# Kernel optimization log

Measured on AMD Instinct MI355X. Metric: run time of the kernel, lower is better.

The kernel has to match this reference:

```python
import jax, jax.numpy as jnp
import numpy as np

EPS = 1e-3  # keras LayerNormalization default epsilon

def _ln(x, gamma, beta):
    m = jnp.mean(x, axis=-1, keepdims=True)
    v = jnp.var(x, axis=-1, keepdims=True)
    return gamma * (x - m) * jax.lax.rsqrt(v + EPS) + beta

def setup_inputs() -> dict:
    B, T, F, H = 256, 128, 4, 512  # T*F must equal H (skip-connection constraint in context GRN)
    D = T * F
    key = jax.random.key(0)
    ks = jax.random.split(key, 16)
    s = lambda fan: 1.0 / np.sqrt(fan)
    inp = {
        "inputs": jax.random.normal(ks[0], (B, T, F), jnp.float32),
        # context GRN (input dim D = T*F = H)
        "W1c": jax.random.normal(ks[1], (D, H), jnp.float32) * s(D),
        "b1c": jnp.zeros((H,), jnp.float32),
        "W2c": jax.random.normal(ks[2], (H, H), jnp.float32) * s(H),
        "b2c": jnp.zeros((H,), jnp.float32),
        "Wgc": jax.random.normal(ks[3], (H, H), jnp.float32) * s(H),
        "bgc": jnp.zeros((H,), jnp.float32),
        "gamma_c": jnp.ones((H,), jnp.float32),
        "beta_c": jnp.zeros((H,), jnp.float32),
        # softmax variable-selection head
        "Wsel": jax.random.normal(ks[4], (H, F), jnp.float32) * s(H),
        "bsel": jnp.zeros((F,), jnp.float32),
        # F per-variable GRNs, batched over leading F axis (input dim 1)
        "w1": jax.random.normal(ks[5], (F, H), jnp.float32),
        "b1": jnp.zeros((F, H), jnp.float32),
        "W2": jax.random.normal(ks[6], (F, H, H), jnp.float32) * s(H),
        "b2": jnp.zeros((F, H), jnp.float32),
        "Wg": jax.random.normal(ks[7], (F, H, H), jnp.float32) * s(H),
        "bg": jnp.zeros((F, H), jnp.float32),
        "gamma": jnp.ones((F, H), jnp.float32),
        "beta": jnp.zeros((F, H), jnp.float32),
    }
    return inp

def reference(inputs, W1c, b1c, W2c, b2c, Wgc, bgc, gamma_c, beta_c,
              Wsel, bsel, w1, b1, W2, b2, Wg, bg, gamma, beta):
    B, T, F = inputs.shape
    # ---- context GRN on flattened inputs (skip == flat since T*F == H) ----
    flat = inputs.reshape(B, T * F)
    x = jax.nn.elu(flat @ W1c + b1c)
    x = x @ W2c + b2c
    g = jax.nn.sigmoid(x @ Wgc + bgc)
    ctx = _ln(g * x + (1.0 - g) * flat, gamma_c, beta_c)
    # ---- softmax selection weights over variables ----
    sel = jax.nn.softmax(ctx @ Wsel + bsel)  # [B, F]
    # ---- per-variable GRNs, batched over F (input is scalar per variable) ----
    v = inputs[..., None]                              # [B,T,F,1] (skip path)
    x1 = jax.nn.elu(v * w1 + b1)                       # [B,T,F,H]
    x2 = jnp.einsum('btfh,fhk->btfk', x1, W2) + b2     # dense2
    gv = jax.nn.sigmoid(jnp.einsum('btfh,fhk->btfk', x2, Wg) + bg)
    gated = gv * x2 + (1.0 - gv) * v                   # skip broadcasts [B,T,F,1]
    tv = _ln(gated, gamma, beta)                       # [B,T,F,H]
    # ---- weighted sum over variables ----
    selected = jnp.einsum('btfh,bf->bth', tv, sel)     # [B,T,H]
    sel_weights = jnp.tile(sel[:, None, None, :], (1, T, 1, 1))  # [B,T,1,F]
    return selected, sel_weights
```

## Files before the change

### kernel.cpp

```cpp
#include <hip/hip_runtime.h>
#include <math.h>


#define H 512
#define NF 4
#define MTOT 32768

typedef unsigned short u16;
typedef unsigned int u32;
typedef __attribute__((ext_vector_type(8))) short short8;
typedef __attribute__((ext_vector_type(4))) float f32x4;
typedef __attribute__((ext_vector_type(4))) u32 u32x4;

__device__ __forceinline__ u16 f2bf(float x) {
  union { float f; u32 u; } v; v.f = x;
  return (u16)((v.u + 0x7fffu + ((v.u >> 16) & 1u)) >> 16);
}
__device__ __forceinline__ float bf2f(u32 h16) {
  union { u32 u; float f; } v; v.u = h16 << 16;
  return v.f;
}
__device__ __forceinline__ float elu_f(float x) {
  return x > 0.0f ? x : (__expf(x) - 1.0f);
}
__device__ __forceinline__ float sigmoid_f(float x) {
  return __builtin_amdgcn_rcpf(1.0f + __expf(-x));
}
__device__ __forceinline__ u32 cvtpk(float lo, float hi) {
  u32 r;
  asm("v_cvt_pk_bf16_f32 %0, %1, %2" : "=v"(r) : "v"(lo), "v"(hi));
  return r;
}
template <int CTRL>
__device__ __forceinline__ float dppadd(float v) {
  int t = __builtin_amdgcn_update_dpp(0, __float_as_int(v), CTRL, 0xF, 0xF, true);
  return v + __int_as_float(t);
}
__device__ __forceinline__ float red16(float v) {
  v = dppadd<0xB1>(v);
  v = dppadd<0x4E>(v);
  v = dppadd<0x141>(v);
  v = dppadd<0x140>(v);
  return v;
}

__device__ __forceinline__ void glld16(const void* g, void* l) {
  __builtin_amdgcn_global_load_lds(
      (const __attribute__((address_space(1))) u32*)(unsigned long long)(uintptr_t)g,
      (__attribute__((address_space(3))) u32*)(u32)(uintptr_t)l, 16, 0, 0);
}

#define MFMA16(a, b, c) __builtin_amdgcn_mfma_f32_16x16x32_bf16((a), (b), (c), 0, 0, 0)

__device__ __forceinline__ int sA_idx(int m, int n) {
  return m * 512 + ((((n >> 3) ^ (m & 7)) << 3) + (n & 7));
}

struct TileCtx {
  int tid, wid, lane, quad, col;
};

__global__ __launch_bounds__(256)
void pack_vsn(const float* __restrict__ W2, const float* __restrict__ Wg,
              u16* __restrict__ W2p, u16* __restrict__ Wgp) {
  int g = blockIdx.x * 256 + threadIdx.x;
  int r = g & 32767; int mat = g >> 15;
  int lane = r & 63, nt = (r >> 6) & 31, kk = (r >> 11) & 15;
  const float* src; u16* dst;
  if (mat < 4) { src = W2 + (size_t)mat * 262144;       dst = W2p + (size_t)mat * 262144; }
  else         { src = Wg + (size_t)(mat - 4) * 262144; dst = Wgp + (size_t)(mat - 4) * 262144; }
  dst += (size_t)r * 8;
  int n  = nt * 16 + (lane & 15);
  int k0 = kk * 32 + (lane >> 4) * 8;
  short8 pk;
  #pragma unroll
  for (int j = 0; j < 8; ++j) pk[j] = (short)f2bf(src[(size_t)(k0 + j) * H + n]);
  *(short8*)dst = pk;
}

__global__ __launch_bounds__(256)
void pack_ctx(const float* __restrict__ W1c, const float* __restrict__ W2c,
              const float* __restrict__ Wgc, u16* __restrict__ Cp) {
  int g = blockIdx.x * 256 + threadIdx.x;
  int r = g & 32767; int mat = g >> 15;
  const float* src = (mat == 0) ? W1c : (mat == 1) ? W2c : Wgc;
  u16* dst = Cp + (size_t)mat * 262144 + (size_t)r * 8;
  int lane = r & 63;
  int n, k0;
  if (mat < 2) {
    int nb = r >> 12, kk = (r >> 8) & 15, ntg = (r >> 6) & 3;
    n  = nb * 64 + ntg * 16 + (lane & 15);
    k0 = kk * 32 + (lane >> 4) * 8;
  } else {
    int nt = (r >> 6) & 31, kk = (r >> 11) & 15;
    n  = nt * 16 + (lane & 15);
    k0 = kk * 32 + (lane >> 4) * 8;
  }
  short8 pk;
  #pragma unroll
  for (int j = 0; j < 8; ++j) pk[j] = (short)f2bf(src[(size_t)(k0 + j) * H + n]);
  *(short8*)dst = pk;
}


__device__ __forceinline__ void slab_kloop(const TileCtx& c, const u16* Wslab,
                                           u16* sA, u16* sB0, u16* sB1,
                                           f32x4 acc[4]) {
  #pragma unroll 1
  for (int kk = 0; kk < 16; ++kk) {
    if (kk < 15)
      glld16(Wslab + (kk + 1) * 2048 + c.tid * 8,
             (((kk + 1) & 1) ? sB1 : sB0) + c.tid * 8);
    const u16* bp = ((kk & 1) ? sB1 : sB0) + c.wid * 512 + c.lane * 8;
    short8 bb = *(const short8*)(bp);
    const int kq = kk * 4 + c.quad;
    const int s0 = (kq ^ (c.col & 7)) * 8;
    short8 a0 = *(const short8*)&sA[(     c.col) * 512 + s0];
    short8 a1 = *(const short8*)&sA[(16 + c.col) * 512 + s0];
    short8 a2 = *(const short8*)&sA[(32 + c.col) * 512 + s0];
    short8 a3 = *(const short8*)&sA[(48 + c.col) * 512 + s0];
    acc[0] = MFMA16(a0, bb, acc[0]);
    acc[1] = MFMA16(a1, bb, acc[1]);
    acc[2] = MFMA16(a2, bb, acc[2]);
    acc[3] = MFMA16(a3, bb, acc[3]);
    __syncthreads();
  }
}

__global__ __launch_bounds__(256)
void ctx_g1(const float* __restrict__ in, const u16* __restrict__ Cp,
            const float* __restrict__ b1c, u16* __restrict__ x1g) {
  __shared__ __align__(16) u16 smem[36864];
  u16* const sA  = smem;
  u16* const sB0 = smem + 32768;
  u16* const sB1 = smem + 34816;
  TileCtx c;
  c.tid = threadIdx.x; c.wid = c.tid >> 6; c.lane = c.tid & 63;
  c.quad = c.lane >> 4; c.col = c.lane & 15;
  const int mb = blockIdx.x >> 3, nb = blockIdx.x & 7;
  const int m0 = mb * 64;
  const u16* Wslab = Cp + (size_t)nb * 32768;

  glld16(Wslab + c.tid * 8, sB0 + c.tid * 8);

  {
    const int m = c.tid >> 2;
    const int kb = (c.tid & 3) * 128;
    const float* rowp = in + (size_t)(m0 + m) * H;
    #pragma unroll
    for (int gg = 0; gg < 16; ++gg) {
      const int ge = (gg + (c.tid & 3) * 4) & 15;
      const int k = kb + ge * 8;
      float4 v0 = *(const float4*)&rowp[k];
      float4 v1 = *(const float4*)&rowp[k + 4];
      u32x4 pk4;
      pk4.x = cvtpk(v0.x, v0.y); pk4.y = cvtpk(v0.z, v0.w);
      pk4.z = cvtpk(v1.x, v1.y); pk4.w = cvtpk(v1.z, v1.w);
      const int grp = (k >> 3) ^ (m & 7);
      *(u32x4*)&sA[m * 512 + grp * 8] = pk4;
    }
  }
  __syncthreads();

  f32x4 acc[4];
  #pragma unroll
  for (int mt = 0; mt < 4; ++mt) acc[mt] = (f32x4){0,0,0,0};
  slab_kloop(c, Wslab, sA, sB0, sB1, acc);

  const int n = nb * 64 + c.wid * 16 + c.col;
  const float bv = b1c[n];
  #pragma unroll
  for (int mt = 0; mt < 4; ++mt)
    #pragma unroll
    for (int reg = 0; reg < 4; ++reg) {
      const int m = m0 + mt * 16 + c.quad * 4 + reg;
      x1g[(size_t)m * H + n] = f2bf(elu_f(acc[mt][reg] + bv));
    }
}

__global__ __launch_bounds__(256)
void ctx_g2(const u16* __restrict__ x1g, const u16* __restrict__ Cp,
            const float* __restrict__ b2c, u16* __restrict__ xg) {
  __shared__ __align__(16) u16 smem[36864];
  u16* const sA  = smem;
  u16* const sB0 = smem + 32768;
  u16* const sB1 = smem + 34816;
  TileCtx c;
  c.tid = threadIdx.x; c.wid = c.tid >> 6; c.lane = c.tid & 63;
  c.quad = c.lane >> 4; c.col = c.lane & 15;
  const int mb = blockIdx.x >> 3, nb = blockIdx.x & 7;
  const int m0 = mb * 64;
  const u16* Wslab = Cp + 262144 + (size_t)nb * 32768;

  glld16(Wslab + c.tid * 8, sB0 + c.tid * 8);

  {
    const int m = c.tid >> 2;
    const int kb = (c.tid & 3) * 128;
    const u16* rowp = x1g + (size_t)(m0 + m) * H;
    #pragma unroll
    for (int gg = 0; gg < 16; ++gg) {
      const int ge = (gg + (c.tid & 3) * 4) & 15;
      const int k = kb + ge * 8;
      short8 w = *(const short8*)&rowp[k];
      const int grp = (k >> 3) ^ (m & 7);
      *(short8*)&sA[m * 512 + grp * 8] = w;
    }
  }
  __syncthreads();

  f32x4 acc[4];
  #pragma unroll
  for (int mt = 0; mt < 4; ++mt) acc[mt] = (f32x4){0,0,0,0};
  slab_kloop(c, Wslab, sA, sB0, sB1, acc);

  const int n = nb * 64 + c.wid * 16 + c.col;
  const float bv = b2c[n];
  #pragma unroll
  for (int mt = 0; mt < 4; ++mt)
    #pragma unroll
    for (int reg = 0; reg < 4; ++reg) {
      const int m = m0 + mt * 16 + c.quad * 4 + reg;
      xg[(size_t)m * H + n] = f2bf(acc[mt][reg] + bv);
    }
}


__device__ __forceinline__ void stage_chunk8(int tid, const u16* src, u16* dst) {
  glld16(src + tid * 8,         dst + tid * 8);
  glld16(src + tid * 8 + 4096,  dst + tid * 8 + 4096);
  glld16(src + tid * 8 + 8192,  dst + tid * 8 + 8192);
  glld16(src + tid * 8 + 12288, dst + tid * 8 + 12288);
}

template <bool PREFETCH_TAIL>
__device__ __forceinline__ void gemm_kloop8(const TileCtx& c, const u16* Wp,
                                            const u16* nextWp,
                                            u16* sA, u16* sB0, u16* sB1,
                                            f32x4 acc[4][4]) {
  #pragma unroll 1
  for (int kk = 0; kk < 16; ++kk) {
    if (kk < 15) {
      stage_chunk8(c.tid, Wp + (kk + 1) * 16384, (((kk + 1) & 1) ? sB1 : sB0));
    } else if (PREFETCH_TAIL) {
      stage_chunk8(c.tid, nextWp, sB0);
    }
    const u16* bp = ((kk & 1) ? sB1 : sB0) + c.wid * 2048 + c.lane * 8;
    short8 bb[4];
    #pragma unroll
    for (int nt = 0; nt < 4; ++nt) bb[nt] = *(const short8*)(bp + nt * 512);
    const int kq = kk * 4 + c.quad;
    const int s0 = (kq ^ (c.col & 7)) * 8;
    #pragma unroll
    for (int mt = 0; mt < 4; ++mt) {
      short8 a = *(const short8*)&sA[(mt * 16 + c.col) * 512 + s0];
      #pragma unroll
      for (int nt = 0; nt < 4; ++nt)
        acc[mt][nt] = MFMA16(a, bb[nt], acc[mt][nt]);
    }
    __syncthreads();
  }
}

__device__ __forceinline__ void store_x2_pair_n(const TileCtx& c, u16* sA,
                                                int mt, int n, u32 o01, u32 o23) {
  const bool even = (c.lane & 1) == 0;
  const u32 send = even ? o23 : o01;
  const u32 recv = (u32)__builtin_amdgcn_update_dpp(0, (int)send, 0xB1, 0xF, 0xF, true);
  const u32 hi = even ? recv : o23;
  const u32 lo = even ? o01 : recv;
  const u32 dlo = __builtin_amdgcn_perm(hi, lo, 0x05040100u);
  const u32 dhi = __builtin_amdgcn_perm(hi, lo, 0x07060302u);
  const int np = n & ~1;
  const int mA = mt * 16 + c.quad * 4 + (even ? 0 : 2);
  const int iA = mA * 512 + ((((np >> 3) ^ (mA & 7)) << 3) + (np & 7));
  const int mB = mA + 1;
  const int iB = mB * 512 + ((((np >> 3) ^ (mB & 7)) << 3) + (np & 7));
  *(u32*)&sA[iA] = dlo;
  *(u32*)&sA[iB] = dhi;
}

__device__ __forceinline__ void ln_reduce8(const TileCtx& c, float* sRedF,
                                           f32x4 acc[4][4]) {
  #pragma unroll
  for (int mt = 0; mt < 4; ++mt) {
    float rs[4], rq[4];
    #pragma unroll
    for (int reg = 0; reg < 4; ++reg) {
      rs[reg] = 0.f; rq[reg] = 0.f;
      #pragma unroll
      for (int nt = 0; nt < 4; ++nt) {
        const float gt = acc[mt][nt][reg];
        rs[reg] += gt; rq[reg] += gt * gt;
      }
      rs[reg] = red16(rs[reg]);
      rq[reg] = red16(rq[reg]);
    }
    if (c.col == 0) {
      #pragma unroll
      for (int reg = 0; reg < 4; ++reg) {
        const int m = mt * 16 + c.quad * 4 + reg;
        float2 sq; sq.x = rs[reg]; sq.y = rq[reg];
        *(float2*)&sRedF[m * 20 + c.wid * 2] = sq;
      }
    }
  }
  __syncthreads();
  if (c.tid < 64) {
    const int row = c.tid;
    float s = 0.f, q = 0.f;
    #pragma unroll
    for (int jj = 0; jj < 4; ++jj) {
      float4 v = *(float4*)&sRedF[row * 20 + jj * 4];
      s += v.x + v.z; q += v.y + v.w;
    }
    const float mu = s * (1.0f / H);
    const float rstd = rsqrtf(q * (1.0f / H) - mu * mu + 1e-3f);
    float2 mr; mr.x = mu; mr.y = rstd;
    *(float2*)&sRedF[1280 + row * 2] = mr;
  }
  __syncthreads();
}

__global__ __launch_bounds__(512)
void ctx_g3(const float* __restrict__ in, const u16* __restrict__ xg,
            const u16* __restrict__ Cp,
            const float* __restrict__ bgc,
            const float* __restrict__ gamma_c, const float* __restrict__ beta_c,
            const float* __restrict__ Wsel, const float* __restrict__ bsel,
            float* __restrict__ sel_ws,
            float* __restrict__ selw_out)
{
  __shared__ __align__(16) u16 smem[65536];
  u16* const sA  = smem;
  u16* const sB0 = smem + 32768;
  u16* const sB1 = smem + 49152;
  float* const sRedF = (float*)sB0;
  float* const sZp   = (float*)sB0 + 2048;
  float* const sZf   = (float*)sB0 + 4096;
  float* const sSel  = (float*)sB0 + 4352;

  TileCtx c;
  c.tid = threadIdx.x; c.wid = c.tid >> 6; c.lane = c.tid & 63;
  c.quad = c.lane >> 4; c.col = c.lane & 15;
  const int b0 = blockIdx.x * 64;
  const u16* Wgcp = Cp + 524288;

  stage_chunk8(c.tid, Wgcp, sB0);

  {
    const int m  = c.tid >> 3;
    const int kb = (c.tid & 7) * 64;
    const u16* rowp = xg + (size_t)(b0 + m) * H;
    #pragma unroll
    for (int gg = 0; gg < 8; ++gg) {
      const int ge = (gg + (c.tid & 7)) & 7;
      const int k = kb + ge * 8;
      short8 w = *(const short8*)&rowp[k];
      const int grp = (k >> 3) ^ (m & 7);
      *(short8*)&sA[m * 512 + grp * 8] = w;
    }
  }
  __syncthreads();

  f32x4 acc[4][4];
  #pragma unroll
  for (int mt = 0; mt < 4; ++mt)
    #pragma unroll
    for (int nt = 0; nt < 4; ++nt) acc[mt][nt] = (f32x4){0,0,0,0};
  gemm_kloop8<false>(c, Wgcp, nullptr, sA, sB0, sB1, acc);

  {
    float bv[4];
    #pragma unroll
    for (int nt = 0; nt < 4; ++nt) bv[nt] = bgc[c.wid * 64 + nt * 16 + c.col];
    #pragma unroll
    for (int mt = 0; mt < 4; ++mt)
      #pragma unroll
      for (int nt = 0; nt < 4; ++nt) {
        const int n = c.wid * 64 + nt * 16 + c.col;
        #pragma unroll
        for (int reg = 0; reg < 4; ++reg) {
          const int m = mt * 16 + c.quad * 4 + reg;
          const float xv = bf2f(sA[sA_idx(m, n)]);
          const float fl = in[(size_t)(b0 + m) * H + n];
          const float gv = sigmoid_f(acc[mt][nt][reg] + bv[nt]);
          acc[mt][nt][reg] = gv * xv + (1.0f - gv) * fl;
        }
      }
  }
  __syncthreads();
  ln_reduce8(c, sRedF, acc);

  {
    float gm[4], bt[4]; float4 ws4[4];
    #pragma unroll
    for (int nt = 0; nt < 4; ++nt) {
      const int n = c.wid * 64 + nt * 16 + c.col;
      gm[nt] = gamma_c[n]; bt[nt] = beta_c[n];
      ws4[nt] = *(const float4*)&Wsel[n * NF];
    }
    #pragma unroll
    for (int mt = 0; mt < 4; ++mt)
      #pragma unroll
      for (int reg = 0; reg < 4; ++reg) {
        const int m = mt * 16 + c.quad * 4 + reg;
        float2 mr = *(float2*)&sRedF[1280 + m * 2];
        float zp[4] = {0.f, 0.f, 0.f, 0.f};
        #pragma unroll
        for (int nt = 0; nt < 4; ++nt) {
          const float ctxv = gm[nt] * ((acc[mt][nt][reg] - mr.x) * mr.y) + bt[nt];
          zp[0] = fmaf(ctxv, ws4[nt].x, zp[0]);
          zp[1] = fmaf(ctxv, ws4[nt].y, zp[1]);
          zp[2] = fmaf(ctxv, ws4[nt].z, zp[2]);
          zp[3] = fmaf(ctxv, ws4[nt].w, zp[3]);
        }
        #pragma unroll
        for (int f = 0; f < 4; ++f) zp[f] = red16(zp[f]);
        if (c.col == 0) {
          #pragma unroll
          for (int f = 0; f < 4; ++f) sZp[(m * 8 + c.wid) * 4 + f] = zp[f];
        }
      }
  }
  __syncthreads();
  if (c.tid < 256) {
    const int m = c.tid >> 2, f = c.tid & 3;
    float z = bsel[f];
    #pragma unroll
    for (int w = 0; w < 8; ++w) z += sZp[(m * 8 + w) * 4 + f];
    sZf[m * 4 + f] = z;
  }
  __syncthreads();
  if (c.tid < 64) {
    const int m = c.tid;
    float z0 = sZf[m*4], z1 = sZf[m*4+1], z2 = sZf[m*4+2], z3 = sZf[m*4+3];
    float mx = fmaxf(fmaxf(z0, z1), fmaxf(z2, z3));
    float e0 = __expf(z0-mx), e1 = __expf(z1-mx), e2 = __expf(z2-mx), e3 = __expf(z3-mx);
    float inv = __builtin_amdgcn_rcpf(e0 + e1 + e2 + e3);
    sSel[m*4]   = e0*inv; sSel[m*4+1] = e1*inv;
    sSel[m*4+2] = e2*inv; sSel[m*4+3] = e3*inv;
    sel_ws[(b0+m)*NF]   = e0*inv; sel_ws[(b0+m)*NF+1] = e1*inv;
    sel_ws[(b0+m)*NF+2] = e2*inv; sel_ws[(b0+m)*NF+3] = e3*inv;
  }
  __syncthreads();
  {
    const int m = c.tid >> 3;
    const int jb = (c.tid & 7) * 64;
    float4 v; v.x = sSel[m*4]; v.y = sSel[m*4+1]; v.z = sSel[m*4+2]; v.w = sSel[m*4+3];
    #pragma unroll
    for (int j = 0; j < 16; ++j)
      *(float4*)&selw_out[(size_t)(b0 + m) * H + jb + j * 4] = v;
  }
}

__global__ __launch_bounds__(512, 2)
void vsn_mfma(const float* __restrict__ in,
              const float* __restrict__ w1, const float* __restrict__ b1,
              const float* __restrict__ b2, const float* __restrict__ bg,
              const float* __restrict__ gamma, const float* __restrict__ beta,
              const u16* __restrict__ W2p, const u16* __restrict__ Wgp,
              const float* __restrict__ sel_ws,
              float* __restrict__ out)
{
  __shared__ __align__(16) u16 smem[65536];
  u16* const sA  = smem;
  u16* const sB0 = smem + 32768;
  u16* const sB1 = smem + 49152;
  float* const sRedF = (float*)smem;

  TileCtx c;
  c.tid = threadIdx.x; c.wid = c.tid >> 6; c.lane = c.tid & 63;
  c.quad = c.lane >> 4; c.col = c.lane & 15;
  const int row0 = blockIdx.x * 64;
  const int bidx = row0 >> 7;

  f32x4 outacc[4][4];
  #pragma unroll
  for (int mt = 0; mt < 4; ++mt)
    #pragma unroll
    for (int nt = 0; nt < 4; ++nt) outacc[mt][nt] = (f32x4){0,0,0,0};

  stage_chunk8(c.tid, W2p, sB0);

  #pragma unroll 1
  for (int f = 0; f < NF; ++f) {
    const u16* W2f = W2p + (size_t)f * 262144;
    const u16* Wgf = Wgp + (size_t)f * 262144;
    const u16* W2n = W2p + (size_t)((f + 1) & 3) * 262144;

    {
      const int m  = c.tid >> 3;
      const int kb = (c.tid & 7) * 64;
      const float v = in[(size_t)(row0 + m) * NF + f];
      const float* w1f = w1 + f * H;
      const float* b1f = b1 + f * H;
      #pragma unroll
      for (int gg = 0; gg < 8; ++gg) {
        const int ge = (gg + (c.tid & 7)) & 7;
        const int k = kb + ge * 8;
        float4 wv0 = *(const float4*)&w1f[k];
        float4 wv1 = *(const float4*)&w1f[k + 4];
        float4 bv0 = *(const float4*)&b1f[k];
        float4 bv1 = *(const float4*)&b1f[k + 4];
        u32x4 pk4;
        pk4.x = cvtpk(elu_f(fmaf(v, wv0.x, bv0.x)), elu_f(fmaf(v, wv0.y, bv0.y)));
        pk4.y = cvtpk(elu_f(fmaf(v, wv0.z, bv0.z)), elu_f(fmaf(v, wv0.w, bv0.w)));
        pk4.z = cvtpk(elu_f(fmaf(v, wv1.x, bv1.x)), elu_f(fmaf(v, wv1.y, bv1.y)));
        pk4.w = cvtpk(elu_f(fmaf(v, wv1.z, bv1.z)), elu_f(fmaf(v, wv1.w, bv1.w)));
        const int grp = (k >> 3) ^ (m & 7);
        *(u32x4*)&sA[m * 512 + grp * 8] = pk4;
      }
    }
    __syncthreads();

    f32x4 acc[4][4];
    #pragma unroll
    for (int mt = 0; mt < 4; ++mt)
      #pragma unroll
      for (int nt = 0; nt < 4; ++nt) acc[mt][nt] = (f32x4){0,0,0,0};

    gemm_kloop8<true>(c, W2f, Wgf, sA, sB0, sB1, acc);

    u32 x2p[4][4][2];
    {
      float bv[4];
      #pragma unroll
      for (int nt = 0; nt < 4; ++nt) bv[nt] = b2[f * H + c.wid * 64 + nt * 16 + c.col];
      #pragma unroll
      for (int mt = 0; mt < 4; ++mt)
        #pragma unroll
        for (int nt = 0; nt < 4; ++nt) {
          const u32 o01 = cvtpk(acc[mt][nt][0] + bv[nt], acc[mt][nt][1] + bv[nt]);
          const u32 o23 = cvtpk(acc[mt][nt][2] + bv[nt], acc[mt][nt][3] + bv[nt]);
          x2p[mt][nt][0] = o01; x2p[mt][nt][1] = o23;
          store_x2_pair_n(c, sA, mt, c.wid * 64 + nt * 16 + c.col, o01, o23);
        }
    }
    __syncthreads();

    #pragma unroll
    for (int mt = 0; mt < 4; ++mt)
      #pragma unroll
      for (int nt = 0; nt < 4; ++nt) acc[mt][nt] = (f32x4){0,0,0,0};
    gemm_kloop8<true>(c, Wgf, W2n, sA, sB0, sB1, acc);

    {
      const float selw = sel_ws[bidx * NF + f];
      float bv[4];
      #pragma unroll
      for (int nt = 0; nt < 4; ++nt) bv[nt] = bg[f * H + c.wid * 64 + nt * 16 + c.col];
      #pragma unroll
      for (int mt = 0; mt < 4; ++mt) {
        float vr[4];
        #pragma unroll
        for (int reg = 0; reg < 4; ++reg)
          vr[reg] = in[(size_t)(row0 + mt * 16 + c.quad * 4 + reg) * NF + f];
        #pragma unroll
        for (int nt = 0; nt < 4; ++nt)
          #pragma unroll
          for (int reg = 0; reg < 4; ++reg) {
            const u32 w = x2p[mt][nt][reg >> 1];
            const float x2v = bf2f((reg & 1) ? (w >> 16) : (w & 0xffffu));
            const float gv = sigmoid_f(acc[mt][nt][reg] + bv[nt]);
            acc[mt][nt][reg] = gv * x2v + (1.0f - gv) * vr[reg];
          }
      }
      ln_reduce8(c, sRedF, acc);
      float gm[4], bt[4];
      #pragma unroll
      for (int nt = 0; nt < 4; ++nt) {
        const int n = f * H + c.wid * 64 + nt * 16 + c.col;
        gm[nt] = gamma[n]; bt[nt] = beta[n];
      }
      #pragma unroll
      for (int mt = 0; mt < 4; ++mt)
        #pragma unroll
        for (int reg = 0; reg < 4; ++reg) {
          const int m = mt * 16 + c.quad * 4 + reg;
          float2 mr = *(float2*)&sRedF[1280 + m * 2];
          #pragma unroll
          for (int nt = 0; nt < 4; ++nt) {
            const float tv = gm[nt] * ((acc[mt][nt][reg] - mr.x) * mr.y) + bt[nt];
            outacc[mt][nt][reg] = fmaf(selw, tv, outacc[mt][nt][reg]);
          }
        }
      __syncthreads();
    }
  }

  #pragma unroll
  for (int mt = 0; mt < 4; ++mt)
    #pragma unroll
    for (int reg = 0; reg < 4; ++reg) {
      const int m = row0 + mt * 16 + c.quad * 4 + reg;
      #pragma unroll
      for (int nt = 0; nt < 4; ++nt)
        out[(size_t)m * H + c.wid * 64 + nt * 16 + c.col] = outacc[mt][nt][reg];
    }
}

extern "C" void kernel_launch(void* const* d_in, const int* in_sizes, int n_in,
                              void* d_out, int out_size, void* d_ws, size_t ws_size,
                              hipStream_t stream) {
  const float* in_     = (const float*)d_in[0];
  const float* W1c     = (const float*)d_in[1];
  const float* b1c     = (const float*)d_in[2];
  const float* W2c     = (const float*)d_in[3];
  const float* b2c     = (const float*)d_in[4];
  const float* Wgc     = (const float*)d_in[5];
  const float* bgc     = (const float*)d_in[6];
  const float* gamma_c = (const float*)d_in[7];
  const float* beta_c  = (const float*)d_in[8];
  const float* Wsel    = (const float*)d_in[9];
  const float* bsel    = (const float*)d_in[10];
  const float* w1      = (const float*)d_in[11];
  const float* b1v     = (const float*)d_in[12];
  const float* W2      = (const float*)d_in[13];
  const float* b2v     = (const float*)d_in[14];
  const float* Wg      = (const float*)d_in[15];
  const float* bgv     = (const float*)d_in[16];
  const float* gma     = (const float*)d_in[17];
  const float* bta     = (const float*)d_in[18];

  float* out_sel = (float*)d_out;
  float* out_w   = (float*)d_out + (size_t)MTOT * H;

  float* sel_ws = (float*)d_ws;
  u16*   W2p    = (u16*)((char*)d_ws + 4096);
  u16*   Wgp    = W2p + (size_t)NF * H * H;
  u16*   Cp     = Wgp + (size_t)NF * H * H;
  u16*   x1g    = Cp + 3 * 262144;
  u16*   xg     = x1g + 131072;

  hipLaunchKernelGGL(pack_ctx, dim3(384), dim3(256), 0, stream,
                     W1c, W2c, Wgc, Cp);
  hipLaunchKernelGGL(pack_vsn, dim3(1024), dim3(256), 0, stream,
                     W2, Wg, W2p, Wgp);
  hipLaunchKernelGGL(ctx_g1, dim3(32), dim3(256), 0, stream,
                     in_, Cp, b1c, x1g);
  hipLaunchKernelGGL(ctx_g2, dim3(32), dim3(256), 0, stream,
                     x1g, Cp, b2c, xg);
  hipLaunchKernelGGL(ctx_g3, dim3(4), dim3(512), 0, stream,
                     in_, xg, Cp, bgc, gamma_c, beta_c, Wsel, bsel,
                     sel_ws, out_w);
  hipLaunchKernelGGL(vsn_mfma, dim3(MTOT / 64), dim3(512), 0, stream,
                     in_, w1, b1v, b2v, bgv, gma, bta, W2p, Wgp, sel_ws, out_sel);
}
```

Baseline: 427.4 us.

## Halve VSN row tile to 32, single-buffer B, raise occupancy, merge pack kernels

The main VSN kernel now handles 32 rows per block instead of 64 and uses a single B staging buffer, cutting shared memory from 128KB to 64KB. Launch bounds go from 2 to 4 blocks per CU. The x2 values are re-read from shared memory instead of being held in registers, and the two weight-packing kernels are merged into one launch. The goal is more occupancy and latency hiding, paid for with half the weight reuse per block (each weight tile is streamed twice as often) and lost double-buffered overlap, since staging now sits between two barriers.

```diff
diff --git a/kernel.cpp b/kernel.cpp
--- a/kernel.cpp
+++ b/kernel.cpp
@@ -61,33 +61,22 @@
 };
 
 __global__ __launch_bounds__(256)
-void pack_vsn(const float* __restrict__ W2, const float* __restrict__ Wg,
-              u16* __restrict__ W2p, u16* __restrict__ Wgp) {
+void pack_all(const float* __restrict__ W2, const float* __restrict__ Wg,
+              const float* __restrict__ W1c, const float* __restrict__ W2c,
+              const float* __restrict__ Wgc,
+              u16* __restrict__ W2p, u16* __restrict__ Wgp, u16* __restrict__ Cp) {
   int g = blockIdx.x * 256 + threadIdx.x;
   int r = g & 32767; int mat = g >> 15;
-  int lane = r & 63, nt = (r >> 6) & 31, kk = (r >> 11) & 15;
+  if (mat >= 11) return;
   const float* src; u16* dst;
-  if (mat < 4) { src = W2 + (size_t)mat * 262144;       dst = W2p + (size_t)mat * 262144; }
-  else         { src = Wg + (size_t)(mat - 4) * 262144; dst = Wgp + (size_t)(mat - 4) * 262144; }
+  if (mat < 4)      { src = W2 + (size_t)mat * 262144;       dst = W2p + (size_t)mat * 262144; }
+  else if (mat < 8) { src = Wg + (size_t)(mat - 4) * 262144; dst = Wgp + (size_t)(mat - 4) * 262144; }
+  else              { src = (mat == 8 ? W1c : (mat == 9 ? W2c : Wgc));
+                      dst = Cp + (size_t)(mat - 8) * 262144; }
   dst += (size_t)r * 8;
-  int n  = nt * 16 + (lane & 15);
-  int k0 = kk * 32 + (lane >> 4) * 8;
-  short8 pk;
-  #pragma unroll
-  for (int j = 0; j < 8; ++j) pk[j] = (short)f2bf(src[(size_t)(k0 + j) * H + n]);
-  *(short8*)dst = pk;
-}
-
-__global__ __launch_bounds__(256)
-void pack_ctx(const float* __restrict__ W1c, const float* __restrict__ W2c,
-              const float* __restrict__ Wgc, u16* __restrict__ Cp) {
-  int g = blockIdx.x * 256 + threadIdx.x;
-  int r = g & 32767; int mat = g >> 15;
-  const float* src = (mat == 0) ? W1c : (mat == 1) ? W2c : Wgc;
-  u16* dst = Cp + (size_t)mat * 262144 + (size_t)r * 8;
   int lane = r & 63;
   int n, k0;
-  if (mat < 2) {
+  if (mat == 8 || mat == 9) {
     int nb = r >> 12, kk = (r >> 8) & 15, ntg = (r >> 6) & 3;
     n  = nb * 64 + ntg * 16 + (lane & 15);
     k0 = kk * 32 + (lane >> 4) * 8;
@@ -101,7 +90,6 @@
   for (int j = 0; j < 8; ++j) pk[j] = (short)f2bf(src[(size_t)(k0 + j) * H + n]);
   *(short8*)dst = pk;
 }
-
 
 __device__ __forceinline__ void slab_kloop(const TileCtx& c, const u16* Wslab,
                                            u16* sA, u16* sB0, u16* sB1,
@@ -262,24 +250,6 @@
   }
 }
 
-__device__ __forceinline__ void store_x2_pair_n(const TileCtx& c, u16* sA,
-                                                int mt, int n, u32 o01, u32 o23) {
-  const bool even = (c.lane & 1) == 0;
-  const u32 send = even ? o23 : o01;
-  const u32 recv = (u32)__builtin_amdgcn_update_dpp(0, (int)send, 0xB1, 0xF, 0xF, true);
-  const u32 hi = even ? recv : o23;
-  const u32 lo = even ? o01 : recv;
-  const u32 dlo = __builtin_amdgcn_perm(hi, lo, 0x05040100u);
-  const u32 dhi = __builtin_amdgcn_perm(hi, lo, 0x07060302u);
-  const int np = n & ~1;
-  const int mA = mt * 16 + c.quad * 4 + (even ? 0 : 2);
-  const int iA = mA * 512 + ((((np >> 3) ^ (mA & 7)) << 3) + (np & 7));
-  const int mB = mA + 1;
-  const int iB = mB * 512 + ((((np >> 3) ^ (mB & 7)) << 3) + (np & 7));
-  *(u32*)&sA[iA] = dlo;
-  *(u32*)&sA[iB] = dhi;
-}
-
 __device__ __forceinline__ void ln_reduce8(const TileCtx& c, float* sRedF,
                                            f32x4 acc[4][4]) {
   #pragma unroll
@@ -454,7 +424,94 @@
   }
 }
 
-__global__ __launch_bounds__(512, 2)
+
+template <bool PREFETCH_TAIL>
+__device__ __forceinline__ void gemm_kloop32(const TileCtx& c, const u16* Wp,
+                                             const u16* nextWp,
+                                             u16* sA, u16* sB,
+                                             f32x4 acc[2][4]) {
+  #pragma unroll 1
+  for (int kk = 0; kk < 16; ++kk) {
+    const u16* bp = sB + c.wid * 2048 + c.lane * 8;
+    short8 bb[4];
+    #pragma unroll
+    for (int nt = 0; nt < 4; ++nt) bb[nt] = *(const short8*)(bp + nt * 512);
+    const int kq = kk * 4 + c.quad;
+    const int s0 = (kq ^ (c.col & 7)) * 8;
+    short8 a0 = *(const short8*)&sA[(     c.col) * 512 + s0];
+    short8 a1 = *(const short8*)&sA[(16 + c.col) * 512 + s0];
+    #pragma unroll
+    for (int nt = 0; nt < 4; ++nt) acc[0][nt] = MFMA16(a0, bb[nt], acc[0][nt]);
+    #pragma unroll
+    for (int nt = 0; nt < 4; ++nt) acc[1][nt] = MFMA16(a1, bb[nt], acc[1][nt]);
+    __syncthreads();
+    if (kk < 15)            stage_chunk8(c.tid, Wp + (kk + 1) * 16384, sB);
+    else if (PREFETCH_TAIL) stage_chunk8(c.tid, nextWp, sB);
+    __syncthreads();
+  }
+}
+
+__device__ __forceinline__ void store_x2_pair_n(const TileCtx& c, u16* sA,
+                                                int mt, int n, u32 o01, u32 o23) {
+  const bool even = (c.lane & 1) == 0;
+  const u32 send = even ? o23 : o01;
+  const u32 recv = (u32)__builtin_amdgcn_update_dpp(0, (int)send, 0xB1, 0xF, 0xF, true);
+  const u32 hi = even ? recv : o23;
+  const u32 lo = even ? o01 : recv;
+  const u32 dlo = __builtin_amdgcn_perm(hi, lo, 0x05040100u);
+  const u32 dhi = __builtin_amdgcn_perm(hi, lo, 0x07060302u);
+  const int np = n & ~1;
+  const int mA = mt * 16 + c.quad * 4 + (even ? 0 : 2);
+  const int iA = mA * 512 + ((((np >> 3) ^ (mA & 7)) << 3) + (np & 7));
+  const int mB = mA + 1;
+  const int iB = mB * 512 + ((((np >> 3) ^ (mB & 7)) << 3) + (np & 7));
+  *(u32*)&sA[iA] = dlo;
+  *(u32*)&sA[iB] = dhi;
+}
+
+__device__ __forceinline__ void ln_reduce32(const TileCtx& c, float* sRedF,
+                                            f32x4 acc[2][4]) {
+  #pragma unroll
+  for (int mt = 0; mt < 2; ++mt) {
+    float rs[4], rq[4];
+    #pragma unroll
+    for (int reg = 0; reg < 4; ++reg) {
+      rs[reg] = 0.f; rq[reg] = 0.f;
+      #pragma unroll
+      for (int nt = 0; nt < 4; ++nt) {
+        const float gt = acc[mt][nt][reg];
+        rs[reg] += gt; rq[reg] += gt * gt;
+      }
+      rs[reg] = red16(rs[reg]);
+      rq[reg] = red16(rq[reg]);
+    }
+    if (c.col == 0) {
+      #pragma unroll
+      for (int reg = 0; reg < 4; ++reg) {
+        const int m = mt * 16 + c.quad * 4 + reg;
+        float2 sq; sq.x = rs[reg]; sq.y = rq[reg];
+        *(float2*)&sRedF[m * 20 + c.wid * 2] = sq;
+      }
+    }
+  }
+  __syncthreads();
+  if (c.tid < 32) {
+    const int row = c.tid;
+    float s = 0.f, q = 0.f;
+    #pragma unroll
+    for (int jj = 0; jj < 4; ++jj) {
+      float4 v = *(float4*)&sRedF[row * 20 + jj * 4];
+      s += v.x + v.z; q += v.y + v.w;
+    }
+    const float mu = s * (1.0f / H);
+    const float rstd = rsqrtf(q * (1.0f / H) - mu * mu + 1e-3f);
+    float2 mr; mr.x = mu; mr.y = rstd;
+    *(float2*)&sRedF[640 + row * 2] = mr;
+  }
+  __syncthreads();
+}
+
+__global__ __launch_bounds__(512, 4)
 void vsn_mfma(const float* __restrict__ in,
               const float* __restrict__ w1, const float* __restrict__ b1,
               const float* __restrict__ b2, const float* __restrict__ bg,
@@ -463,25 +520,24 @@
               const float* __restrict__ sel_ws,
               float* __restrict__ out)
 {
-  __shared__ __align__(16) u16 smem[65536];
-  u16* const sA  = smem;
-  u16* const sB0 = smem + 32768;
-  u16* const sB1 = smem + 49152;
+  __shared__ __align__(16) u16 smem[32768];
+  u16* const sA = smem;
+  u16* const sB = smem + 16384;
   float* const sRedF = (float*)smem;
 
   TileCtx c;
   c.tid = threadIdx.x; c.wid = c.tid >> 6; c.lane = c.tid & 63;
   c.quad = c.lane >> 4; c.col = c.lane & 15;
-  const int row0 = blockIdx.x * 64;
+  const int row0 = blockIdx.x * 32;
   const int bidx = row0 >> 7;
 
-  f32x4 outacc[4][4];
-  #pragma unroll
-  for (int mt = 0; mt < 4; ++mt)
+  f32x4 outacc[2][4];
+  #pragma unroll
+  for (int mt = 0; mt < 2; ++mt)
     #pragma unroll
     for (int nt = 0; nt < 4; ++nt) outacc[mt][nt] = (f32x4){0,0,0,0};
 
-  stage_chunk8(c.tid, W2p, sB0);
+  stage_chunk8(c.tid, W2p, sB);
 
   #pragma unroll 1
   for (int f = 0; f < NF; ++f) {
@@ -490,14 +546,14 @@
     const u16* W2n = W2p + (size_t)((f + 1) & 3) * 262144;
 
     {
-      const int m  = c.tid >> 3;
-      const int kb = (c.tid & 7) * 64;
+      const int m  = c.tid >> 4;
+      const int kb = (c.tid & 15) * 32;
       const float v = in[(size_t)(row0 + m) * NF + f];
       const float* w1f = w1 + f * H;
       const float* b1f = b1 + f * H;
       #pragma unroll
-      for (int gg = 0; gg < 8; ++gg) {
-        const int ge = (gg + (c.tid & 7)) & 7;
+      for (int gg = 0; gg < 4; ++gg) {
+        const int ge = (gg + (c.tid & 15)) & 3;
         const int k = kb + ge * 8;
         float4 wv0 = *(const float4*)&w1f[k];
         float4 wv1 = *(const float4*)&w1f[k + 4];
@@ -514,36 +570,34 @@
     }
     __syncthreads();
 
-    f32x4 acc[4][4];
-    #pragma unroll
-    for (int mt = 0; mt < 4; ++mt)
+    f32x4 acc[2][4];
+    #pragma unroll
+    for (int mt = 0; mt < 2; ++mt)
       #pragma unroll
       for (int nt = 0; nt < 4; ++nt) acc[mt][nt] = (f32x4){0,0,0,0};
 
-    gemm_kloop8<true>(c, W2f, Wgf, sA, sB0, sB1, acc);
-
-    u32 x2p[4][4][2];
+    gemm_kloop32<true>(c, W2f, Wgf, sA, sB, acc);
+
     {
       float bv[4];
       #pragma unroll
       for (int nt = 0; nt < 4; ++nt) bv[nt] = b2[f * H + c.wid * 64 + nt * 16 + c.col];
       #pragma unroll
-      for (int mt = 0; mt < 4; ++mt)
+      for (int mt = 0; mt < 2; ++mt)
         #pragma unroll
         for (int nt = 0; nt < 4; ++nt) {
           const u32 o01 = cvtpk(acc[mt][nt][0] + bv[nt], acc[mt][nt][1] + bv[nt]);
           const u32 o23 = cvtpk(acc[mt][nt][2] + bv[nt], acc[mt][nt][3] + bv[nt]);
-          x2p[mt][nt][0] = o01; x2p[mt][nt][1] = o23;
           store_x2_pair_n(c, sA, mt, c.wid * 64 + nt * 16 + c.col, o01, o23);
         }
     }
     __syncthreads();
 
     #pragma unroll
-    for (int mt = 0; mt < 4; ++mt)
+    for (int mt = 0; mt < 2; ++mt)
       #pragma unroll
       for (int nt = 0; nt < 4; ++nt) acc[mt][nt] = (f32x4){0,0,0,0};
-    gemm_kloop8<true>(c, Wgf, W2n, sA, sB0, sB1, acc);
+    gemm_kloop32<true>(c, Wgf, W2n, sA, sB, acc);
 
     {
       const float selw = sel_ws[bidx * NF + f];
@@ -551,22 +605,25 @@
       #pragma unroll
       for (int nt = 0; nt < 4; ++nt) bv[nt] = bg[f * H + c.wid * 64 + nt * 16 + c.col];
       #pragma unroll
-      for (int mt = 0; mt < 4; ++mt) {
+      for (int mt = 0; mt < 2; ++mt) {
         float vr[4];
         #pragma unroll
         for (int reg = 0; reg < 4; ++reg)
           vr[reg] = in[(size_t)(row0 + mt * 16 + c.quad * 4 + reg) * NF + f];
         #pragma unroll
-        for (int nt = 0; nt < 4; ++nt)
+        for (int nt = 0; nt < 4; ++nt) {
+          const int n = c.wid * 64 + nt * 16 + c.col;
           #pragma unroll
           for (int reg = 0; reg < 4; ++reg) {
-            const u32 w = x2p[mt][nt][reg >> 1];
-            const float x2v = bf2f((reg & 1) ? (w >> 16) : (w & 0xffffu));
+            const int m = mt * 16 + c.quad * 4 + reg;
+            const float x2v = bf2f(sA[sA_idx(m, n)]);
             const float gv = sigmoid_f(acc[mt][nt][reg] + bv[nt]);
             acc[mt][nt][reg] = gv * x2v + (1.0f - gv) * vr[reg];
           }
-      }
-      ln_reduce8(c, sRedF, acc);
+        }
+      }
+      __syncthreads();
+      ln_reduce32(c, sRedF, acc);
       float gm[4], bt[4];
       #pragma unroll
       for (int nt = 0; nt < 4; ++nt) {
@@ -574,11 +631,11 @@
         gm[nt] = gamma[n]; bt[nt] = beta[n];
       }
       #pragma unroll
-      for (int mt = 0; mt < 4; ++mt)
+      for (int mt = 0; mt < 2; ++mt)
         #pragma unroll
         for (int reg = 0; reg < 4; ++reg) {
           const int m = mt * 16 + c.quad * 4 + reg;
-          float2 mr = *(float2*)&sRedF[1280 + m * 2];
+          float2 mr = *(float2*)&sRedF[640 + m * 2];
           #pragma unroll
           for (int nt = 0; nt < 4; ++nt) {
             const float tv = gm[nt] * ((acc[mt][nt][reg] - mr.x) * mr.y) + bt[nt];
@@ -590,7 +647,7 @@
   }
 
   #pragma unroll
-  for (int mt = 0; mt < 4; ++mt)
+  for (int mt = 0; mt < 2; ++mt)
     #pragma unroll
     for (int reg = 0; reg < 4; ++reg) {
       const int m = row0 + mt * 16 + c.quad * 4 + reg;
@@ -633,10 +690,8 @@
   u16*   x1g    = Cp + 3 * 262144;
   u16*   xg     = x1g + 131072;
 
-  hipLaunchKernelGGL(pack_ctx, dim3(384), dim3(256), 0, stream,
-                     W1c, W2c, Wgc, Cp);
-  hipLaunchKernelGGL(pack_vsn, dim3(1024), dim3(256), 0, stream,
-                     W2, Wg, W2p, Wgp);
+  hipLaunchKernelGGL(pack_all, dim3(1408), dim3(256), 0, stream,
+                     W2, Wg, W1c, W2c, Wgc, W2p, Wgp, Cp);
   hipLaunchKernelGGL(ctx_g1, dim3(32), dim3(256), 0, stream,
                      in_, Cp, b1c, x1g);
   hipLaunchKernelGGL(ctx_g2, dim3(32), dim3(256), 0, stream,
@@ -644,6 +699,6 @@
   hipLaunchKernelGGL(ctx_g3, dim3(4), dim3(512), 0, stream,
                      in_, xg, Cp, bgc, gamma_c, beta_c, Wsel, bsel,
                      sel_ws, out_w);
-  hipLaunchKernelGGL(vsn_mfma, dim3(MTOT / 64), dim3(512), 0, stream,
+  hipLaunchKernelGGL(vsn_mfma, dim3(MTOT / 32), dim3(512), 0, stream,
                      in_, w1, b1v, b2v, bgv, gma, bta, W2p, Wgp, sel_ws, out_sel);
 }
```

Result: slower. 549.7 us (+28.6%).
